# Optimization experiments

Hardware: AMD Instinct MI355X
Metric: run time of the kernel (lower is better)

Reference implementation:

```python
import jax, jax.numpy as jnp
import numpy as np

GROUPS = 4
EPS = 1e-5


def _distill(x, fc1_w, fc1_b, ln_w, ln_b, fc2_w, fc2_b):
    # x: [N, cs, H, W] -> gated x (the 'input * gate' output of ChannelGate_sub)
    p = x.mean(axis=(2, 3))                     # global avg pool -> [N, cs]
    p = p @ fc1_w.T + fc1_b                     # 1x1 conv == dense on pooled vec
    mu = p.mean(axis=-1, keepdims=True)         # LayerNorm over [cs,1,1] == over channel dim
    var = jnp.mean((p - mu) ** 2, axis=-1, keepdims=True)
    p = (p - mu) * jax.lax.rsqrt(var + EPS) * ln_w + ln_b
    p = jax.nn.relu(p)
    p = p @ fc2_w.T + fc2_b
    g = jax.nn.sigmoid(p)                       # [N, cs]
    return x * g[:, :, None, None]


def _forward(x, cweight, cbias, sweight, sbias, gn_w, gn_b,
             fc1_w, fc1_b, ln_w, ln_b, fc2_w, fc2_b):
    b, c, h, w = x.shape
    x = x.reshape(b * GROUPS, c // GROUPS, h, w)
    cs = c // (2 * GROUPS)
    x0, x1 = x[:, :cs], x[:, cs:]               # chunk(2, dim=1)

    # channel-attention branch
    xn = x0.mean(axis=(2, 3), keepdims=True)    # [N, cs, 1, 1]
    xn = cweight * xn + cbias
    xn = x0 * jax.nn.sigmoid(xn)
    x_reid_0 = x0 - xn
    xn = xn + _distill(x_reid_0, fc1_w, fc1_b, ln_w, ln_b, fc2_w, fc2_b)

    # spatial-attention branch: GroupNorm(cs groups, cs channels) == per-channel instance norm
    mu = x1.mean(axis=(2, 3), keepdims=True)
    var = jnp.mean((x1 - mu) ** 2, axis=(2, 3), keepdims=True)
    xs = (x1 - mu) * jax.lax.rsqrt(var + EPS)
    xs = xs * gn_w[None, :, None, None] + gn_b[None, :, None, None]
    xs = sweight * xs + sbias
    xs = x1 * jax.nn.sigmoid(xs)
    x_reid_1 = x1 - xs
    xs = xs + _distill(x_reid_1, fc1_w, fc1_b, ln_w, ln_b, fc2_w, fc2_b)

    out = jnp.concatenate([xn, xs], axis=1)
    return out.reshape(b, c, h, w)


def setup_inputs() -> dict:
    key = jax.random.key(0)
    ks = jax.random.split(key, 14)
    B, C, H, W = 32, 256, 64, 64
    cs = C // (2 * GROUPS)  # 32
    s = 0.1
    return {
        "x": jax.random.normal(ks[0], (B, C, H, W), jnp.float32),
        "cweight": jax.random.normal(ks[1], (1, cs, 1, 1), jnp.float32) * s,
        "cbias": jnp.ones((1, cs, 1, 1), jnp.float32) + jax.random.normal(ks[2], (1, cs, 1, 1), jnp.float32) * s,
        "sweight": jax.random.normal(ks[3], (1, cs, H, W), jnp.float32) * s,
        "sbias": jnp.ones((1, cs, 1, 1), jnp.float32) + jax.random.normal(ks[4], (1, cs, 1, 1), jnp.float32) * s,
        "gn_w": jnp.ones((cs,), jnp.float32) + jax.random.normal(ks[5], (cs,), jnp.float32) * s,
        "gn_b": jax.random.normal(ks[6], (cs,), jnp.float32) * s,
        "fc1_w": jax.random.normal(ks[7], (cs, cs), jnp.float32) * (1.0 / np.sqrt(cs)),
        "fc1_b": jax.random.normal(ks[8], (cs,), jnp.float32) * s,
        "ln_w": jnp.ones((cs,), jnp.float32) + jax.random.normal(ks[9], (cs,), jnp.float32) * s,
        "ln_b": jax.random.normal(ks[10], (cs,), jnp.float32) * s,
        "fc2_w": jax.random.normal(ks[11], (cs, cs), jnp.float32) * (1.0 / np.sqrt(cs)),
        "fc2_b": jax.random.normal(ks[12], (cs,), jnp.float32) * s,
    }


def reference(x, cweight, cbias, sweight, sbias, gn_w, gn_b,
              fc1_w, fc1_b, ln_w, ln_b, fc2_w, fc2_b):
    return _forward(x, cweight, cbias, sweight, sbias, gn_w, gn_b,
                    fc1_w, fc1_b, ln_w, ln_b, fc2_w, fc2_b)
```

## Files before the change

### kernel.cpp

```cpp
#include <hip/hip_runtime.h>
#include <math.h>

#define HW 4096
#define CS 32
#define NS 128
#define NPLANES 8192
#define EPS 1e-5f
#define SENT 0x7F7F7F7Fu

__device__ __forceinline__ float sigmoidf_(float x) {
    return 1.0f / (1.0f + __expf(-x));
}

__global__ __launch_bounds__(256) void fused_sentinel(
    const float* __restrict__ x, float* __restrict__ out,
    const float* __restrict__ cw,  const float* __restrict__ cb,
    const float* __restrict__ sw,  const float* __restrict__ sb,
    const float* __restrict__ gnw, const float* __restrict__ gnb,
    const float* __restrict__ fc1w, const float* __restrict__ fc1b,
    const float* __restrict__ lnw, const float* __restrict__ lnb,
    const float* __restrict__ fc2w, const float* __restrict__ fc2b,
    unsigned int* __restrict__ pvbuf) {
    const int P = blockIdx.x;
    const int cc = P & 63;
    const int branch = cc >> 5;
    const int c = cc & 31;
    const int tid = threadIdx.x;
    const int wave = tid >> 6, lane = tid & 63;

    __shared__ float ls[4], ls2[4];
    __shared__ float bcmu, bcrs, bcg0, bcsc;

    const float4* xp = (const float4*)x + (size_t)P * 1024;
    float4 v[4];
    float s = 0.f, s2 = 0.f;
#pragma unroll
    for (int k = 0; k < 4; ++k) {
        v[k] = xp[tid + k * 256];
        s  += v[k].x + v[k].y + v[k].z + v[k].w;
        s2 += v[k].x * v[k].x + v[k].y * v[k].y
            + v[k].z * v[k].z + v[k].w * v[k].w;
    }
#pragma unroll
    for (int k = 0; k < 4; ++k)
        asm volatile("" : "+v"(v[k].x), "+v"(v[k].y), "+v"(v[k].z), "+v"(v[k].w));

    for (int off = 32; off; off >>= 1) {
        s  += __shfl_down(s,  off, 64);
        s2 += __shfl_down(s2, off, 64);
    }
    if (lane == 0) { ls[wave] = s; ls2[wave] = s2; }
    __syncthreads();

    if (branch == 0) {
        if (tid == 0) {
            float mean = (ls[0] + ls[1] + ls[2] + ls[3]) * (1.0f / HW);
            float g0 = sigmoidf_(cw[c] * mean + cb[c]);
            bcg0 = g0;
            float pv = mean * (1.0f - g0);
            __hip_atomic_store(&pvbuf[P], __float_as_uint(pv),
                               __ATOMIC_RELAXED, __HIP_MEMORY_SCOPE_AGENT);
        }
    } else {
        if (tid == 0) {
            float mu  = (ls[0] + ls[1] + ls[2] + ls[3]) * (1.0f / HW);
            float var = (ls2[0] + ls2[1] + ls2[2] + ls2[3]) * (1.0f / HW) - mu * mu;
            bcmu = mu;
            bcrs = rsqrtf(var + EPS);
        }
        __syncthreads();
        const float mu = bcmu, rs = bcrs;
        const float a   = gnw[c] * rs;
        const float b0  = gnb[c] - mu * a;
        const float sbv = sb[c];
        const float4* wp = (const float4*)sw + (size_t)c * 1024;
        float sx = 0.f;
#pragma unroll
        for (int k = 0; k < 4; ++k) {
            float4 w = wp[tid + k * 256];
            sx += v[k].x * sigmoidf_(w.x * (v[k].x * a + b0) + sbv);
            sx += v[k].y * sigmoidf_(w.y * (v[k].y * a + b0) + sbv);
            sx += v[k].z * sigmoidf_(w.z * (v[k].z * a + b0) + sbv);
            sx += v[k].w * sigmoidf_(w.w * (v[k].w * a + b0) + sbv);
        }
        for (int off = 32; off; off >>= 1) sx += __shfl_down(sx, off, 64);
        if (lane == 0) ls[wave] = sx;
        __syncthreads();
        if (tid == 0) {
            float sxt = ls[0] + ls[1] + ls[2] + ls[3];
            float pv = bcmu - sxt * (1.0f / HW);
            __hip_atomic_store(&pvbuf[P], __float_as_uint(pv),
                               __ATOMIC_RELAXED, __HIP_MEMORY_SCOPE_AGENT);
        }
    }

    if (wave == 0) {
        const int l = lane & 31;
        const unsigned int* slot = &pvbuf[(P & ~31) + l];
        unsigned int bits = __hip_atomic_load(slot, __ATOMIC_RELAXED,
                                              __HIP_MEMORY_SCOPE_AGENT);
        int spins = 0;
        while (__any(bits == SENT) && ++spins < (1 << 18)) {
            __builtin_amdgcn_s_sleep(2);
            bits = __hip_atomic_load(slot, __ATOMIC_RELAXED,
                                     __HIP_MEMORY_SCOPE_AGENT);
        }
        float pv = __uint_as_float(bits);

        float qv = fc1b[l];
#pragma unroll 8
        for (int j = 0; j < CS; ++j)
            qv += fc1w[l * CS + j] * __shfl(pv, (lane & 32) + j, 64);
        float bs = qv, bs2 = qv * qv;
        for (int m = 1; m < 32; m <<= 1) {
            bs  += __shfl_xor(bs,  m, 64);
            bs2 += __shfl_xor(bs2, m, 64);
        }
        float mu  = bs * (1.0f / CS);
        float var = bs2 * (1.0f / CS) - mu * mu;
        float r   = fmaxf((qv - mu) * rsqrtf(var + EPS) * lnw[l] + lnb[l], 0.f);
        float sv  = fc2b[l];
#pragma unroll 8
        for (int j = 0; j < CS; ++j)
            sv += fc2w[l * CS + j] * __shfl(r, (lane & 32) + j, 64);
        float gd  = sigmoidf_(sv);
        float gdc = __shfl(gd, c, 64);
        if (tid == 0) bcsc = branch ? gdc : (bcg0 + (1.0f - bcg0) * gdc);
    }
    __syncthreads();

    const float sc = bcsc;
    float4* op = (float4*)out + (size_t)P * 1024;
    if (branch == 0) {
#pragma unroll
        for (int k = 0; k < 4; ++k) {
            float4 o = v[k];
            o.x *= sc; o.y *= sc; o.z *= sc; o.w *= sc;
            op[tid + k * 256] = o;
        }
    } else {
        const float mu = bcmu, rs = bcrs;
        const float a   = gnw[c] * rs;
        const float b0  = gnb[c] - mu * a;
        const float sbv = sb[c];
        const float4* wp = (const float4*)sw + (size_t)c * 1024;
#pragma unroll
        for (int k = 0; k < 4; ++k) {
            float4 w = wp[tid + k * 256];
            float4 o; float sg;
            sg = sigmoidf_(w.x * (v[k].x * a + b0) + sbv); o.x = v[k].x * (sg + (1.f - sg) * sc);
            sg = sigmoidf_(w.y * (v[k].y * a + b0) + sbv); o.y = v[k].y * (sg + (1.f - sg) * sc);
            sg = sigmoidf_(w.z * (v[k].z * a + b0) + sbv); o.z = v[k].z * (sg + (1.f - sg) * sc);
            sg = sigmoidf_(w.w * (v[k].w * a + b0) + sbv); o.w = v[k].w * (sg + (1.f - sg) * sc);
            op[tid + k * 256] = o;
        }
    }
}

extern "C" void kernel_launch(void* const* d_in, const int* in_sizes, int n_in,
                              void* d_out, int out_size, void* d_ws, size_t ws_size,
                              hipStream_t stream) {
    const float* x    = (const float*)d_in[0];
    const float* cw   = (const float*)d_in[1];
    const float* cb   = (const float*)d_in[2];
    const float* sw   = (const float*)d_in[3];
    const float* sb   = (const float*)d_in[4];
    const float* gnw  = (const float*)d_in[5];
    const float* gnb  = (const float*)d_in[6];
    const float* fc1w = (const float*)d_in[7];
    const float* fc1b = (const float*)d_in[8];
    const float* lnw  = (const float*)d_in[9];
    const float* lnb  = (const float*)d_in[10];
    const float* fc2w = (const float*)d_in[11];
    const float* fc2b = (const float*)d_in[12];
    float* out = (float*)d_out;

    unsigned int* pvbuf = (unsigned int*)d_ws;

    hipMemsetAsync(pvbuf, 0x7F, NPLANES * sizeof(unsigned int), stream);
    fused_sentinel<<<NPLANES, 256, 0, stream>>>(x, out, cw, cb, sw, sb,
                                                gnw, gnb, fc1w, fc1b,
                                                lnw, lnb, fc2w, fc2b, pvbuf);
}
```

Baseline: 81.21 us.

## Process both branch planes of a channel pair in one block

Each block now loads and handles the channel-attention plane and the spatial-attention plane for the same channel index and group, halving the grid to 4096 blocks. The two branches' pooled values are published to the shared buffer, and wave 0 waits on all 64 slots of the group to compute both distill gates at once. This evens out per-block work between the light and heavy branches and gives each thread more independent loads in flight. In exchange it doubles per-thread register use for the held data, which may lower occupancy.

```diff
diff --git a/kernel.cpp b/kernel.cpp
--- a/kernel.cpp
+++ b/kernel.cpp
@@ -4,7 +4,7 @@
 #define HW 4096
 #define CS 32
 #define NS 128
-#define NPLANES 8192
+#define NBLK 4096
 #define EPS 1e-5f
 #define SENT 0x7F7F7F7Fu
 
@@ -12,7 +12,7 @@
     return 1.0f / (1.0f + __expf(-x));
 }
 
-__global__ __launch_bounds__(256) void fused_sentinel(
+__global__ __launch_bounds__(256) void fused_pair(
     const float* __restrict__ x, float* __restrict__ out,
     const float* __restrict__ cw,  const float* __restrict__ cb,
     const float* __restrict__ sw,  const float* __restrict__ sb,
@@ -21,82 +21,84 @@
     const float* __restrict__ lnw, const float* __restrict__ lnb,
     const float* __restrict__ fc2w, const float* __restrict__ fc2b,
     unsigned int* __restrict__ pvbuf) {
-    const int P = blockIdx.x;
-    const int cc = P & 63;
-    const int branch = cc >> 5;
-    const int c = cc & 31;
+    const int B = blockIdx.x;
+    const int n = B >> 5, c = B & 31;
     const int tid = threadIdx.x;
     const int wave = tid >> 6, lane = tid & 63;
 
-    __shared__ float ls[4], ls2[4];
-    __shared__ float bcmu, bcrs, bcg0, bcsc;
+    __shared__ float lsA[4], lsB[4], lsC[4];
+    __shared__ float bcmu, bcrs, bcg0, bcsc0, bcsc1;
 
-    const float4* xp = (const float4*)x + (size_t)P * 1024;
-    float4 v[4];
-    float s = 0.f, s2 = 0.f;
+    const float4* xp0 = (const float4*)x + (size_t)(n * 64 + c) * 1024;
+    const float4* xp1 = (const float4*)x + (size_t)(n * 64 + CS + c) * 1024;
+
+    float4 v0[4], v1[4];
+#pragma unroll
+    for (int k = 0; k < 4; ++k) { v0[k] = xp0[tid + k * 256]; v1[k] = xp1[tid + k * 256]; }
 #pragma unroll
     for (int k = 0; k < 4; ++k) {
-        v[k] = xp[tid + k * 256];
-        s  += v[k].x + v[k].y + v[k].z + v[k].w;
-        s2 += v[k].x * v[k].x + v[k].y * v[k].y
-            + v[k].z * v[k].z + v[k].w * v[k].w;
+        asm volatile("" : "+v"(v0[k].x), "+v"(v0[k].y), "+v"(v0[k].z), "+v"(v0[k].w));
+        asm volatile("" : "+v"(v1[k].x), "+v"(v1[k].y), "+v"(v1[k].z), "+v"(v1[k].w));
     }
+    float s0 = 0.f, s1 = 0.f, q1 = 0.f;
 #pragma unroll
-    for (int k = 0; k < 4; ++k)
-        asm volatile("" : "+v"(v[k].x), "+v"(v[k].y), "+v"(v[k].z), "+v"(v[k].w));
-
+    for (int k = 0; k < 4; ++k) {
+        s0 += v0[k].x + v0[k].y + v0[k].z + v0[k].w;
+        s1 += v1[k].x + v1[k].y + v1[k].z + v1[k].w;
+        q1 += v1[k].x * v1[k].x + v1[k].y * v1[k].y
+            + v1[k].z * v1[k].z + v1[k].w * v1[k].w;
+    }
     for (int off = 32; off; off >>= 1) {
-        s  += __shfl_down(s,  off, 64);
-        s2 += __shfl_down(s2, off, 64);
+        s0 += __shfl_down(s0, off, 64);
+        s1 += __shfl_down(s1, off, 64);
+        q1 += __shfl_down(q1, off, 64);
     }
-    if (lane == 0) { ls[wave] = s; ls2[wave] = s2; }
+    if (lane == 0) { lsA[wave] = s0; lsB[wave] = s1; lsC[wave] = q1; }
+    __syncthreads();
+    if (tid == 0) {
+        float sum0 = lsA[0] + lsA[1] + lsA[2] + lsA[3];
+        float sum1 = lsB[0] + lsB[1] + lsB[2] + lsB[3];
+        float sq1  = lsC[0] + lsC[1] + lsC[2] + lsC[3];
+        float mean0 = sum0 * (1.0f / HW);
+        float g0 = sigmoidf_(cw[c] * mean0 + cb[c]);
+        bcg0 = g0;
+        __hip_atomic_store(&pvbuf[n * 64 + c],
+                           __float_as_uint(mean0 * (1.0f - g0)),
+                           __ATOMIC_RELAXED, __HIP_MEMORY_SCOPE_AGENT);
+        float mu  = sum1 * (1.0f / HW);
+        float var = sq1 * (1.0f / HW) - mu * mu;
+        bcmu = mu;
+        bcrs = rsqrtf(var + EPS);
+    }
     __syncthreads();
 
-    if (branch == 0) {
-        if (tid == 0) {
-            float mean = (ls[0] + ls[1] + ls[2] + ls[3]) * (1.0f / HW);
-            float g0 = sigmoidf_(cw[c] * mean + cb[c]);
-            bcg0 = g0;
-            float pv = mean * (1.0f - g0);
-            __hip_atomic_store(&pvbuf[P], __float_as_uint(pv),
-                               __ATOMIC_RELAXED, __HIP_MEMORY_SCOPE_AGENT);
-        }
-    } else {
-        if (tid == 0) {
-            float mu  = (ls[0] + ls[1] + ls[2] + ls[3]) * (1.0f / HW);
-            float var = (ls2[0] + ls2[1] + ls2[2] + ls2[3]) * (1.0f / HW) - mu * mu;
-            bcmu = mu;
-            bcrs = rsqrtf(var + EPS);
-        }
-        __syncthreads();
-        const float mu = bcmu, rs = bcrs;
-        const float a   = gnw[c] * rs;
-        const float b0  = gnb[c] - mu * a;
-        const float sbv = sb[c];
-        const float4* wp = (const float4*)sw + (size_t)c * 1024;
-        float sx = 0.f;
+    const float mu = bcmu, rs = bcrs;
+    const float a   = gnw[c] * rs;
+    const float b0  = gnb[c] - mu * a;
+    const float sbv = sb[c];
+    const float4* wp = (const float4*)sw + (size_t)c * 1024;
+    float sx = 0.f;
 #pragma unroll
-        for (int k = 0; k < 4; ++k) {
-            float4 w = wp[tid + k * 256];
-            sx += v[k].x * sigmoidf_(w.x * (v[k].x * a + b0) + sbv);
-            sx += v[k].y * sigmoidf_(w.y * (v[k].y * a + b0) + sbv);
-            sx += v[k].z * sigmoidf_(w.z * (v[k].z * a + b0) + sbv);
-            sx += v[k].w * sigmoidf_(w.w * (v[k].w * a + b0) + sbv);
-        }
-        for (int off = 32; off; off >>= 1) sx += __shfl_down(sx, off, 64);
-        if (lane == 0) ls[wave] = sx;
-        __syncthreads();
-        if (tid == 0) {
-            float sxt = ls[0] + ls[1] + ls[2] + ls[3];
-            float pv = bcmu - sxt * (1.0f / HW);
-            __hip_atomic_store(&pvbuf[P], __float_as_uint(pv),
-                               __ATOMIC_RELAXED, __HIP_MEMORY_SCOPE_AGENT);
-        }
+    for (int k = 0; k < 4; ++k) {
+        float4 w = wp[tid + k * 256];
+        sx += v1[k].x * sigmoidf_(w.x * (v1[k].x * a + b0) + sbv);
+        sx += v1[k].y * sigmoidf_(w.y * (v1[k].y * a + b0) + sbv);
+        sx += v1[k].z * sigmoidf_(w.z * (v1[k].z * a + b0) + sbv);
+        sx += v1[k].w * sigmoidf_(w.w * (v1[k].w * a + b0) + sbv);
+    }
+    for (int off = 32; off; off >>= 1) sx += __shfl_down(sx, off, 64);
+    if (lane == 0) lsA[wave] = sx;
+    __syncthreads();
+    if (tid == 0) {
+        float sxt = lsA[0] + lsA[1] + lsA[2] + lsA[3];
+        __hip_atomic_store(&pvbuf[n * 64 + CS + c],
+                           __float_as_uint(mu - sxt * (1.0f / HW)),
+                           __ATOMIC_RELAXED, __HIP_MEMORY_SCOPE_AGENT);
     }
 
     if (wave == 0) {
         const int l = lane & 31;
-        const unsigned int* slot = &pvbuf[(P & ~31) + l];
+        const unsigned int* slot = &pvbuf[n * 64 + lane];
         unsigned int bits = __hip_atomic_load(slot, __ATOMIC_RELAXED,
                                               __HIP_MEMORY_SCOPE_AGENT);
         int spins = 0;
@@ -116,44 +118,41 @@
             bs  += __shfl_xor(bs,  m, 64);
             bs2 += __shfl_xor(bs2, m, 64);
         }
-        float mu  = bs * (1.0f / CS);
-        float var = bs2 * (1.0f / CS) - mu * mu;
-        float r   = fmaxf((qv - mu) * rsqrtf(var + EPS) * lnw[l] + lnb[l], 0.f);
-        float sv  = fc2b[l];
+        float muq  = bs * (1.0f / CS);
+        float varq = bs2 * (1.0f / CS) - muq * muq;
+        float r    = fmaxf((qv - muq) * rsqrtf(varq + EPS) * lnw[l] + lnb[l], 0.f);
+        float sv   = fc2b[l];
 #pragma unroll 8
         for (int j = 0; j < CS; ++j)
             sv += fc2w[l * CS + j] * __shfl(r, (lane & 32) + j, 64);
         float gd  = sigmoidf_(sv);
-        float gdc = __shfl(gd, c, 64);
-        if (tid == 0) bcsc = branch ? gdc : (bcg0 + (1.0f - bcg0) * gdc);
+        float gd0 = __shfl(gd, c, 64);
+        float gd1 = __shfl(gd, CS + c, 64);
+        if (tid == 0) {
+            bcsc0 = bcg0 + (1.0f - bcg0) * gd0;
+            bcsc1 = gd1;
+        }
     }
     __syncthreads();
 
-    const float sc = bcsc;
-    float4* op = (float4*)out + (size_t)P * 1024;
-    if (branch == 0) {
+    const float sc0 = bcsc0, sc1 = bcsc1;
+    float4* op0 = (float4*)out + (size_t)(n * 64 + c) * 1024;
+    float4* op1 = (float4*)out + (size_t)(n * 64 + CS + c) * 1024;
 #pragma unroll
-        for (int k = 0; k < 4; ++k) {
-            float4 o = v[k];
-            o.x *= sc; o.y *= sc; o.z *= sc; o.w *= sc;
-            op[tid + k * 256] = o;
-        }
-    } else {
-        const float mu = bcmu, rs = bcrs;
-        const float a   = gnw[c] * rs;
-        const float b0  = gnb[c] - mu * a;
-        const float sbv = sb[c];
-        const float4* wp = (const float4*)sw + (size_t)c * 1024;
+    for (int k = 0; k < 4; ++k) {
+        float4 o = v0[k];
+        o.x *= sc0; o.y *= sc0; o.z *= sc0; o.w *= sc0;
+        op0[tid + k * 256] = o;
+    }
 #pragma unroll
-        for (int k = 0; k < 4; ++k) {
-            float4 w = wp[tid + k * 256];
-            float4 o; float sg;
-            sg = sigmoidf_(w.x * (v[k].x * a + b0) + sbv); o.x = v[k].x * (sg + (1.f - sg) * sc);
-            sg = sigmoidf_(w.y * (v[k].y * a + b0) + sbv); o.y = v[k].y * (sg + (1.f - sg) * sc);
-            sg = sigmoidf_(w.z * (v[k].z * a + b0) + sbv); o.z = v[k].z * (sg + (1.f - sg) * sc);
-            sg = sigmoidf_(w.w * (v[k].w * a + b0) + sbv); o.w = v[k].w * (sg + (1.f - sg) * sc);
-            op[tid + k * 256] = o;
-        }
+    for (int k = 0; k < 4; ++k) {
+        float4 w = wp[tid + k * 256];
+        float4 o; float sg;
+        sg = sigmoidf_(w.x * (v1[k].x * a + b0) + sbv); o.x = v1[k].x * (sg + (1.f - sg) * sc1);
+        sg = sigmoidf_(w.y * (v1[k].y * a + b0) + sbv); o.y = v1[k].y * (sg + (1.f - sg) * sc1);
+        sg = sigmoidf_(w.z * (v1[k].z * a + b0) + sbv); o.z = v1[k].z * (sg + (1.f - sg) * sc1);
+        sg = sigmoidf_(w.w * (v1[k].w * a + b0) + sbv); o.w = v1[k].w * (sg + (1.f - sg) * sc1);
+        op1[tid + k * 256] = o;
     }
 }
 
@@ -177,8 +176,8 @@
 
     unsigned int* pvbuf = (unsigned int*)d_ws;
 
-    hipMemsetAsync(pvbuf, 0x7F, NPLANES * sizeof(unsigned int), stream);
-    fused_sentinel<<<NPLANES, 256, 0, stream>>>(x, out, cw, cb, sw, sb,
-                                                gnw, gnb, fc1w, fc1b,
-                                                lnw, lnb, fc2w, fc2b, pvbuf);
+    hipMemsetAsync(pvbuf, 0x7F, 8192 * sizeof(unsigned int), stream);
+    fused_pair<<<NBLK, 256, 0, stream>>>(x, out, cw, cb, sw, sb,
+                                         gnw, gnb, fc1w, fc1b,
+                                         lnw, lnb, fc2w, fc2b, pvbuf);
 }
```

Result: faster. 76.03 us (-6.4%).

## Software-pipeline stats and output phases across blocks with a fixed block lag

Applied to the files above, without the earlier changes.

Each block now computes statistics for plane B and then writes the output for plane B-256, using global sentinel slots to pass per-plane mean, rstd and pooled values between blocks. This removes the in-block spin-wait on sibling planes, since the producers of a lagged plane have likely already finished. The cost is that x (and sweight for branch 1) is read twice instead of being kept in registers, which adds HBM/L2 traffic. It also adds 256 extra blocks and a larger memset.

```diff
diff --git a/kernel.cpp b/kernel.cpp
--- a/kernel.cpp
+++ b/kernel.cpp
@@ -3,8 +3,9 @@
 
 #define HW 4096
 #define CS 32
-#define NS 128
 #define NPLANES 8192
+#define DELTA 256
+#define GRID (NPLANES + DELTA)
 #define EPS 1e-5f
 #define SENT 0x7F7F7F7Fu
 
@@ -12,7 +13,7 @@
     return 1.0f / (1.0f + __expf(-x));
 }
 
-__global__ __launch_bounds__(256) void fused_sentinel(
+__global__ __launch_bounds__(256) void pipe_kernel(
     const float* __restrict__ x, float* __restrict__ out,
     const float* __restrict__ cw,  const float* __restrict__ cb,
     const float* __restrict__ sw,  const float* __restrict__ sb,
@@ -20,139 +21,168 @@
     const float* __restrict__ fc1w, const float* __restrict__ fc1b,
     const float* __restrict__ lnw, const float* __restrict__ lnb,
     const float* __restrict__ fc2w, const float* __restrict__ fc2b,
-    unsigned int* __restrict__ pvbuf) {
-    const int P = blockIdx.x;
-    const int cc = P & 63;
-    const int branch = cc >> 5;
-    const int c = cc & 31;
+    unsigned int* __restrict__ pv, unsigned int* __restrict__ mus,
+    unsigned int* __restrict__ rss) {
+    const int B = blockIdx.x;
     const int tid = threadIdx.x;
     const int wave = tid >> 6, lane = tid & 63;
 
     __shared__ float ls[4], ls2[4];
-    __shared__ float bcmu, bcrs, bcg0, bcsc;
-
-    const float4* xp = (const float4*)x + (size_t)P * 1024;
-    float4 v[4];
-    float s = 0.f, s2 = 0.f;
-#pragma unroll
-    for (int k = 0; k < 4; ++k) {
-        v[k] = xp[tid + k * 256];
-        s  += v[k].x + v[k].y + v[k].z + v[k].w;
-        s2 += v[k].x * v[k].x + v[k].y * v[k].y
-            + v[k].z * v[k].z + v[k].w * v[k].w;
+    __shared__ float bcmu, bcrs;
+    __shared__ float shSc, shMu, shRs;
+
+    if (B < NPLANES) {
+        const int P = B, cc = P & 63, branch = cc >> 5, c = cc & 31;
+        const float4* xp = (const float4*)x + (size_t)P * 1024;
+        if (branch == 0) {
+            float s = 0.f;
+#pragma unroll
+            for (int k = 0; k < 4; ++k) {
+                float4 v = xp[tid + k * 256];
+                s += v.x + v.y + v.z + v.w;
+            }
+            for (int off = 32; off; off >>= 1) s += __shfl_down(s, off, 64);
+            if (lane == 0) ls[wave] = s;
+            __syncthreads();
+            if (tid == 0) {
+                float mean = (ls[0] + ls[1] + ls[2] + ls[3]) * (1.0f / HW);
+                float g0 = sigmoidf_(cw[c] * mean + cb[c]);
+                __hip_atomic_store(&mus[P], __float_as_uint(mean),
+                                   __ATOMIC_RELAXED, __HIP_MEMORY_SCOPE_AGENT);
+                __hip_atomic_store(&pv[P], __float_as_uint(mean * (1.0f - g0)),
+                                   __ATOMIC_RELAXED, __HIP_MEMORY_SCOPE_AGENT);
+            }
+        } else {
+            float4 v[4];
+            float s = 0.f, s2 = 0.f;
+#pragma unroll
+            for (int k = 0; k < 4; ++k) {
+                v[k] = xp[tid + k * 256];
+                s  += v[k].x + v[k].y + v[k].z + v[k].w;
+                s2 += v[k].x * v[k].x + v[k].y * v[k].y
+                    + v[k].z * v[k].z + v[k].w * v[k].w;
+            }
+            for (int off = 32; off; off >>= 1) {
+                s  += __shfl_down(s,  off, 64);
+                s2 += __shfl_down(s2, off, 64);
+            }
+            if (lane == 0) { ls[wave] = s; ls2[wave] = s2; }
+            __syncthreads();
+            if (tid == 0) {
+                float mu  = (ls[0] + ls[1] + ls[2] + ls[3]) * (1.0f / HW);
+                float var = (ls2[0] + ls2[1] + ls2[2] + ls2[3]) * (1.0f / HW) - mu * mu;
+                float rs  = rsqrtf(var + EPS);
+                bcmu = mu; bcrs = rs;
+                __hip_atomic_store(&mus[P], __float_as_uint(mu),
+                                   __ATOMIC_RELAXED, __HIP_MEMORY_SCOPE_AGENT);
+                __hip_atomic_store(&rss[P], __float_as_uint(rs),
+                                   __ATOMIC_RELAXED, __HIP_MEMORY_SCOPE_AGENT);
+            }
+            __syncthreads();
+            const float mu = bcmu, rs = bcrs;
+            const float a   = gnw[c] * rs;
+            const float b0  = gnb[c] - mu * a;
+            const float sbv = sb[c];
+            const float4* wp = (const float4*)sw + (size_t)c * 1024;
+            float sx = 0.f;
+#pragma unroll
+            for (int k = 0; k < 4; ++k) {
+                float4 w = wp[tid + k * 256];
+                sx += v[k].x * sigmoidf_(w.x * (v[k].x * a + b0) + sbv);
+                sx += v[k].y * sigmoidf_(w.y * (v[k].y * a + b0) + sbv);
+                sx += v[k].z * sigmoidf_(w.z * (v[k].z * a + b0) + sbv);
+                sx += v[k].w * sigmoidf_(w.w * (v[k].w * a + b0) + sbv);
+            }
+            for (int off = 32; off; off >>= 1) sx += __shfl_down(sx, off, 64);
+            if (lane == 0) ls[wave] = sx;
+            __syncthreads();
+            if (tid == 0) {
+                float sxt = ls[0] + ls[1] + ls[2] + ls[3];
+                __hip_atomic_store(&pv[P], __float_as_uint(mu - sxt * (1.0f / HW)),
+                                   __ATOMIC_RELAXED, __HIP_MEMORY_SCOPE_AGENT);
+            }
+        }
     }
-#pragma unroll
-    for (int k = 0; k < 4; ++k)
-        asm volatile("" : "+v"(v[k].x), "+v"(v[k].y), "+v"(v[k].z), "+v"(v[k].w));
-
-    for (int off = 32; off; off >>= 1) {
-        s  += __shfl_down(s,  off, 64);
-        s2 += __shfl_down(s2, off, 64);
-    }
-    if (lane == 0) { ls[wave] = s; ls2[wave] = s2; }
-    __syncthreads();
-
-    if (branch == 0) {
-        if (tid == 0) {
-            float mean = (ls[0] + ls[1] + ls[2] + ls[3]) * (1.0f / HW);
-            float g0 = sigmoidf_(cw[c] * mean + cb[c]);
-            bcg0 = g0;
-            float pv = mean * (1.0f - g0);
-            __hip_atomic_store(&pvbuf[P], __float_as_uint(pv),
-                               __ATOMIC_RELAXED, __HIP_MEMORY_SCOPE_AGENT);
-        }
-    } else {
-        if (tid == 0) {
-            float mu  = (ls[0] + ls[1] + ls[2] + ls[3]) * (1.0f / HW);
-            float var = (ls2[0] + ls2[1] + ls2[2] + ls2[3]) * (1.0f / HW) - mu * mu;
-            bcmu = mu;
-            bcrs = rsqrtf(var + EPS);
+
+    if (B >= DELTA) {
+        const int P = B - DELTA, cc = P & 63, branch = cc >> 5, c = cc & 31;
+
+        if (wave == 0) {
+            const int l = lane & 31;
+            const unsigned int* slot =
+                (lane < 32) ? &pv[(P & ~31) + l] :
+                (lane == 32) ? &mus[P] :
+                (lane == 33) ? &rss[P] : &mus[P];
+            const bool active = (lane < 34) && !(lane == 33 && branch == 0);
+            unsigned int bits = 0;
+            if (active) bits = __hip_atomic_load(slot, __ATOMIC_RELAXED,
+                                                 __HIP_MEMORY_SCOPE_AGENT);
+            int spins = 0;
+            while (__any(active && bits == SENT) && ++spins < (1 << 20)) {
+                __builtin_amdgcn_s_sleep(2);
+                if (active) bits = __hip_atomic_load(slot, __ATOMIC_RELAXED,
+                                                     __HIP_MEMORY_SCOPE_AGENT);
+            }
+            float pvv = __uint_as_float(bits);
+
+            float qv = fc1b[l];
+#pragma unroll 8
+            for (int j = 0; j < CS; ++j)
+                qv += fc1w[l * CS + j] * __shfl(pvv, j, 64);
+            float bs = qv, bs2 = qv * qv;
+            for (int m = 1; m < 32; m <<= 1) {
+                bs  += __shfl_xor(bs,  m, 64);
+                bs2 += __shfl_xor(bs2, m, 64);
+            }
+            float muq  = bs * (1.0f / CS);
+            float varq = bs2 * (1.0f / CS) - muq * muq;
+            float r    = fmaxf((qv - muq) * rsqrtf(varq + EPS) * lnw[l] + lnb[l], 0.f);
+            float sv   = fc2b[l];
+#pragma unroll 8
+            for (int j = 0; j < CS; ++j)
+                sv += fc2w[l * CS + j] * __shfl(r, j, 64);
+            float gd  = sigmoidf_(sv);
+            float gdc = __shfl(gd, c, 64);
+            float muP = __uint_as_float((unsigned int)__shfl((int)bits, 32, 64));
+            float rsP = __uint_as_float((unsigned int)__shfl((int)bits, 33, 64));
+            if (lane == 0) {
+                if (branch == 0) {
+                    float g0 = sigmoidf_(cw[c] * muP + cb[c]);
+                    shSc = g0 + (1.0f - g0) * gdc;
+                } else {
+                    shSc = gdc; shMu = muP; shRs = rsP;
+                }
+            }
         }
         __syncthreads();
-        const float mu = bcmu, rs = bcrs;
-        const float a   = gnw[c] * rs;
-        const float b0  = gnb[c] - mu * a;
-        const float sbv = sb[c];
-        const float4* wp = (const float4*)sw + (size_t)c * 1024;
-        float sx = 0.f;
-#pragma unroll
-        for (int k = 0; k < 4; ++k) {
-            float4 w = wp[tid + k * 256];
-            sx += v[k].x * sigmoidf_(w.x * (v[k].x * a + b0) + sbv);
-            sx += v[k].y * sigmoidf_(w.y * (v[k].y * a + b0) + sbv);
-            sx += v[k].z * sigmoidf_(w.z * (v[k].z * a + b0) + sbv);
-            sx += v[k].w * sigmoidf_(w.w * (v[k].w * a + b0) + sbv);
-        }
-        for (int off = 32; off; off >>= 1) sx += __shfl_down(sx, off, 64);
-        if (lane == 0) ls[wave] = sx;
-        __syncthreads();
-        if (tid == 0) {
-            float sxt = ls[0] + ls[1] + ls[2] + ls[3];
-            float pv = bcmu - sxt * (1.0f / HW);
-            __hip_atomic_store(&pvbuf[P], __float_as_uint(pv),
-                               __ATOMIC_RELAXED, __HIP_MEMORY_SCOPE_AGENT);
-        }
-    }
-
-    if (wave == 0) {
-        const int l = lane & 31;
-        const unsigned int* slot = &pvbuf[(P & ~31) + l];
-        unsigned int bits = __hip_atomic_load(slot, __ATOMIC_RELAXED,
-                                              __HIP_MEMORY_SCOPE_AGENT);
-        int spins = 0;
-        while (__any(bits == SENT) && ++spins < (1 << 18)) {
-            __builtin_amdgcn_s_sleep(2);
-            bits = __hip_atomic_load(slot, __ATOMIC_RELAXED,
-                                     __HIP_MEMORY_SCOPE_AGENT);
-        }
-        float pv = __uint_as_float(bits);
-
-        float qv = fc1b[l];
-#pragma unroll 8
-        for (int j = 0; j < CS; ++j)
-            qv += fc1w[l * CS + j] * __shfl(pv, (lane & 32) + j, 64);
-        float bs = qv, bs2 = qv * qv;
-        for (int m = 1; m < 32; m <<= 1) {
-            bs  += __shfl_xor(bs,  m, 64);
-            bs2 += __shfl_xor(bs2, m, 64);
-        }
-        float mu  = bs * (1.0f / CS);
-        float var = bs2 * (1.0f / CS) - mu * mu;
-        float r   = fmaxf((qv - mu) * rsqrtf(var + EPS) * lnw[l] + lnb[l], 0.f);
-        float sv  = fc2b[l];
-#pragma unroll 8
-        for (int j = 0; j < CS; ++j)
-            sv += fc2w[l * CS + j] * __shfl(r, (lane & 32) + j, 64);
-        float gd  = sigmoidf_(sv);
-        float gdc = __shfl(gd, c, 64);
-        if (tid == 0) bcsc = branch ? gdc : (bcg0 + (1.0f - bcg0) * gdc);
-    }
-    __syncthreads();
-
-    const float sc = bcsc;
-    float4* op = (float4*)out + (size_t)P * 1024;
-    if (branch == 0) {
-#pragma unroll
-        for (int k = 0; k < 4; ++k) {
-            float4 o = v[k];
-            o.x *= sc; o.y *= sc; o.z *= sc; o.w *= sc;
-            op[tid + k * 256] = o;
-        }
-    } else {
-        const float mu = bcmu, rs = bcrs;
-        const float a   = gnw[c] * rs;
-        const float b0  = gnb[c] - mu * a;
-        const float sbv = sb[c];
-        const float4* wp = (const float4*)sw + (size_t)c * 1024;
-#pragma unroll
-        for (int k = 0; k < 4; ++k) {
-            float4 w = wp[tid + k * 256];
-            float4 o; float sg;
-            sg = sigmoidf_(w.x * (v[k].x * a + b0) + sbv); o.x = v[k].x * (sg + (1.f - sg) * sc);
-            sg = sigmoidf_(w.y * (v[k].y * a + b0) + sbv); o.y = v[k].y * (sg + (1.f - sg) * sc);
-            sg = sigmoidf_(w.z * (v[k].z * a + b0) + sbv); o.z = v[k].z * (sg + (1.f - sg) * sc);
-            sg = sigmoidf_(w.w * (v[k].w * a + b0) + sbv); o.w = v[k].w * (sg + (1.f - sg) * sc);
-            op[tid + k * 256] = o;
+
+        const float4* xp = (const float4*)x + (size_t)P * 1024;
+        float4* op = (float4*)out + (size_t)P * 1024;
+        if (branch == 0) {
+            const float sc = shSc;
+#pragma unroll
+            for (int k = 0; k < 4; ++k) {
+                float4 o = xp[tid + k * 256];
+                o.x *= sc; o.y *= sc; o.z *= sc; o.w *= sc;
+                op[tid + k * 256] = o;
+            }
+        } else {
+            const float sc = shSc, mu = shMu, rs = shRs;
+            const float a   = gnw[c] * rs;
+            const float b0  = gnb[c] - mu * a;
+            const float sbv = sb[c];
+            const float4* wp = (const float4*)sw + (size_t)c * 1024;
+#pragma unroll
+            for (int k = 0; k < 4; ++k) {
+                float4 v = xp[tid + k * 256];
+                float4 w = wp[tid + k * 256];
+                float4 o; float sg;
+                sg = sigmoidf_(w.x * (v.x * a + b0) + sbv); o.x = v.x * (sg + (1.f - sg) * sc);
+                sg = sigmoidf_(w.y * (v.y * a + b0) + sbv); o.y = v.y * (sg + (1.f - sg) * sc);
+                sg = sigmoidf_(w.z * (v.z * a + b0) + sbv); o.z = v.z * (sg + (1.f - sg) * sc);
+                sg = sigmoidf_(w.w * (v.w * a + b0) + sbv); o.w = v.w * (sg + (1.f - sg) * sc);
+                op[tid + k * 256] = o;
+            }
         }
     }
 }
@@ -175,10 +205,13 @@
     const float* fc2b = (const float*)d_in[12];
     float* out = (float*)d_out;
 
-    unsigned int* pvbuf = (unsigned int*)d_ws;
-
-    hipMemsetAsync(pvbuf, 0x7F, NPLANES * sizeof(unsigned int), stream);
-    fused_sentinel<<<NPLANES, 256, 0, stream>>>(x, out, cw, cb, sw, sb,
-                                                gnw, gnb, fc1w, fc1b,
-                                                lnw, lnb, fc2w, fc2b, pvbuf);
+    unsigned int* pv  = (unsigned int*)d_ws;
+    unsigned int* mus = pv  + NPLANES;
+    unsigned int* rss = mus + NPLANES;
+
+    hipMemsetAsync(pv, 0x7F, 3 * NPLANES * sizeof(unsigned int), stream);
+    pipe_kernel<<<GRID, 256, 0, stream>>>(x, out, cw, cb, sw, sb,
+                                          gnw, gnb, fc1w, fc1b,
+                                          lnw, lnb, fc2w, fc2b,
+                                          pv, mus, rss);
 }
```

New measurement: 76.57 us. 5.7% less time.
